# Performance work log

Hardware: AMD Instinct MI355X
Metric: run time of the kernel (lower is better)

The kernel has to match this reference:

```python
import jax, jax.numpy as jnp
import numpy as np

CODEBOOK_SIZE = 1024
EMBEDDING_DIM = 256
COMMITMENT_COST = 0.25


def setup_inputs() -> dict:
    key = jax.random.key(0)
    k1, k2 = jax.random.split(key)
    x = jax.random.normal(k1, (32, EMBEDDING_DIM, 32, 32), dtype=jnp.float32)
    # embedding initialized uniform(-1/K, 1/K) like the torch module
    embedding = jax.random.uniform(
        k2, (CODEBOOK_SIZE, EMBEDDING_DIM), dtype=jnp.float32,
        minval=-1.0 / CODEBOOK_SIZE, maxval=1.0 / CODEBOOK_SIZE)
    return {"x": x, "embedding": embedding}


def reference(x, embedding):
    # x: [B, C, H, W] -> inputs: [B, H, W, C]
    inputs = jnp.transpose(x, (0, 2, 3, 1))
    input_shape = inputs.shape
    flat = inputs.reshape(-1, EMBEDDING_DIM)  # [N, D]
    # squared L2 distances to codebook: [N, K]
    distances = (jnp.sum(flat ** 2, axis=1, keepdims=True)
                 + jnp.sum(embedding ** 2, axis=1)
                 - 2.0 * flat @ embedding.T)
    encoding_indices = jnp.argmin(distances, axis=1)  # [N]
    encodings = jax.nn.one_hot(encoding_indices, CODEBOOK_SIZE, dtype=jnp.float32)  # [N, K]
    # gather (same math as encodings @ embedding)
    quantized = embedding[encoding_indices].reshape(input_shape)  # [B, H, W, C]
    e_latent_loss = jnp.mean((jax.lax.stop_gradient(quantized) - inputs) ** 2)
    q_latent_loss = jnp.mean((quantized - jax.lax.stop_gradient(inputs)) ** 2)
    loss = q_latent_loss + COMMITMENT_COST * e_latent_loss
    # straight-through estimator
    quantized_st = inputs + jax.lax.stop_gradient(quantized - inputs)
    return (loss, jnp.transpose(quantized_st, (0, 3, 1, 2)), encodings)
```

## Files before the change

kernel.cpp:

```cpp
#include <hip/hip_runtime.h>
#include <cstdint>
#include <cstddef>

constexpr int B = 32, C = 256, H = 32, W = 32;
constexpr int NPTS = B * H * W;
constexpr int DIM  = 256;
constexpr int K    = 1024;
constexpr int QELEMS = B * C * H * W;
constexpr int CHW = C * H * W;

typedef __attribute__((ext_vector_type(8))) short s8v;
typedef __attribute__((ext_vector_type(4))) float f32x4;

#define GLD_LDS16(g, l)                                                        \
  __builtin_amdgcn_global_load_lds(                                            \
      (const __attribute__((address_space(1))) unsigned int*)(g),              \
      (__attribute__((address_space(3))) unsigned int*)(l), 16, 0, 0)

__device__ __forceinline__ unsigned short f2bf(float f) {
  unsigned u = __float_as_uint(f);
  return (unsigned short)((u + 0x7FFFu + ((u >> 16) & 1u)) >> 16);
}

__global__ __launch_bounds__(256) void eprep_kernel(const float* __restrict__ emb,
                                                    unsigned short* __restrict__ ehi,
                                                    float* __restrict__ esq) {
  __shared__ float sums[4][64];
  const int t = threadIdx.x;
  const int k = blockIdx.x * 64 + (t & 63);
  const int seg = t >> 6;
  const float* er = emb + (size_t)k * DIM + seg * 64;
  float v[64];
  float4* v4 = (float4*)v;
#pragma unroll
  for (int i = 0; i < 16; ++i) v4[i] = *(const float4*)(er + i * 4);
  float s = 0.f;
#pragma unroll
  for (int i = 0; i < 64; ++i) s = fmaf(v[i], v[i], s);
  unsigned short* eo = ehi + (size_t)k * DIM + seg * 64;
#pragma unroll
  for (int i = 0; i < 8; ++i) {
    unsigned short h[8];
#pragma unroll
    for (int j = 0; j < 8; ++j) h[j] = f2bf(v[i * 8 + j]);
    *(s8v*)(eo + i * 8) = *(s8v*)h;
  }
  sums[seg][t & 63] = s;
  __syncthreads();
  if (t < 64)
    esq[blockIdx.x * 64 + t] =
        ((sums[0][t] + sums[1][t]) + sums[2][t]) + sums[3][t];
}

__global__ __launch_bounds__(256) void xprep_kernel(const float* __restrict__ x,
                                                    unsigned short* __restrict__ xhi,
                                                    float* __restrict__ xsq) {
  __shared__ float xls[DIM][64];
  const int t = threadIdx.x;
  const int n0 = blockIdx.x * 64;
  const int bb = n0 >> 10, hw0 = n0 & 1023;
  const int p = t & 63, cs = t >> 6;
  const float* xb = x + (size_t)bb * CHW + hw0;
#pragma unroll 8
  for (int r = 0; r < 64; ++r) {
    const int c = r * 4 + cs;
    xls[c][p] = xb[(size_t)c * 1024 + p];
  }
  __syncthreads();
  if (t < 64) {
    float s = 0.f;
#pragma unroll 8
    for (int c = 0; c < 256; ++c) {
      const float v = xls[c][t];
      s = fmaf(v, v, s);
    }
    xsq[n0 + t] = s;
  }
  const int p2 = t >> 2, cb = (t & 3) * 64;
  unsigned short* xo = xhi + (size_t)(n0 + p2) * DIM + cb;
#pragma unroll
  for (int i = 0; i < 8; ++i) {
    unsigned short h[8];
#pragma unroll
    for (int j = 0; j < 8; ++j) h[j] = f2bf(xls[cb + i * 8 + j][p2]);
    *(s8v*)(xo + i * 8) = *(s8v*)h;
  }
}

constexpr float MARGIN = 1e-3f;
__global__ __launch_bounds__(256) void coarse_kernel(
    const unsigned short* __restrict__ xhi, const unsigned short* __restrict__ ehi,
    const float* __restrict__ esq, const float* __restrict__ xsq,
    float* __restrict__ part, unsigned int* __restrict__ cand) {
  __shared__ __align__(16) unsigned short xs[128][32];
  __shared__ __align__(16) unsigned short es[128][32];
  __shared__ float xsq_s[128], esq_s[128], thr_s[128];
  __shared__ unsigned long long red2[2][128];
  __shared__ unsigned int cntL[128];

  const int t = threadIdx.x;
  const int lane = t & 63, w = t >> 6;
  const int wn = (w & 1) * 64, wk = (w >> 1) * 64;
  const int col = lane & 15, quad = lane >> 4;
  const int nblk = blockIdx.x * 128;
  const int kblk = blockIdx.y * 128;

  if (t < 128) {
    xsq_s[t] = xsq[nblk + t];
    esq_s[t] = esq[kblk + t];
    cntL[t] = 0u;
  }

  f32x4 acc[4][4];
#pragma unroll
  for (int i = 0; i < 4; ++i)
#pragma unroll
    for (int j = 0; j < 4; ++j) acc[i][j] = (f32x4){0.f, 0.f, 0.f, 0.f};

  const int gl_row = lane >> 2;
  const int gl_c   = (lane & 3) * 8;

  for (int c0 = 0; c0 < DIM; c0 += 32) {
    __syncthreads();
#pragma unroll
    for (int i = 0; i < 2; ++i) {
      const int inst = w + 4 * i;
      const int row = inst * 16 + gl_row;
      GLD_LDS16(xhi + (size_t)(nblk + row) * DIM + c0 + gl_c, &xs[inst * 16][0]);
      GLD_LDS16(ehi + (size_t)(kblk + row) * DIM + c0 + gl_c, &es[inst * 16][0]);
    }
    __syncthreads();
    s8v a[4], b[4];
#pragma unroll
    for (int ti = 0; ti < 4; ++ti)
      a[ti] = *(const s8v*)&xs[wn + ti * 16 + col][quad * 8];
#pragma unroll
    for (int tj = 0; tj < 4; ++tj)
      b[tj] = *(const s8v*)&es[wk + tj * 16 + col][quad * 8];
#pragma unroll
    for (int ti = 0; ti < 4; ++ti)
#pragma unroll
      for (int tj = 0; tj < 4; ++tj)
        acc[ti][tj] = __builtin_amdgcn_mfma_f32_16x16x32_bf16(
            a[ti], b[tj], acc[ti][tj], 0, 0, 0);
  }

  unsigned long long nmin[4][4];
#pragma unroll
  for (int ti = 0; ti < 4; ++ti)
#pragma unroll
    for (int r = 0; r < 4; ++r) nmin[ti][r] = ~0ULL;
#pragma unroll
  for (int ti = 0; ti < 4; ++ti)
#pragma unroll
    for (int tj = 0; tj < 4; ++tj) {
      const int krel = wk + tj * 16 + col;
      const float eq = esq_s[krel];
#pragma unroll
      for (int r = 0; r < 4; ++r) {
        const int nl = wn + ti * 16 + quad * 4 + r;
        const float d = (xsq_s[nl] + eq) - 2.f * acc[ti][tj][r];
        const unsigned long long key =
            ((unsigned long long)__float_as_uint(d) << 32) |
            (unsigned)(kblk + krel);
        if (key < nmin[ti][r]) nmin[ti][r] = key;
      }
    }
#pragma unroll
  for (int o = 1; o < 16; o <<= 1)
#pragma unroll
    for (int ti = 0; ti < 4; ++ti)
#pragma unroll
      for (int r = 0; r < 4; ++r) {
        const unsigned long long v = __shfl_xor(nmin[ti][r], o, 64);
        if (v < nmin[ti][r]) nmin[ti][r] = v;
      }
  if (col == 0) {
#pragma unroll
    for (int ti = 0; ti < 4; ++ti)
#pragma unroll
      for (int r = 0; r < 4; ++r)
        red2[w >> 1][wn + ti * 16 + quad * 4 + r] = nmin[ti][r];
  }
  __syncthreads();
  if (t < 128) {
    const unsigned long long m0 = red2[0][t], m1 = red2[1][t];
    const unsigned long long m = (m1 < m0) ? m1 : m0;
    const float dmin = __uint_as_float((unsigned)(m >> 32));
    part[(size_t)(nblk + t) * 8 + blockIdx.y] = dmin;
    thr_s[t] = dmin + MARGIN;
  }
  __syncthreads();
#pragma unroll
  for (int ti = 0; ti < 4; ++ti)
#pragma unroll
    for (int tj = 0; tj < 4; ++tj) {
      const int krel = wk + tj * 16 + col;
      const float eq = esq_s[krel];
#pragma unroll
      for (int r = 0; r < 4; ++r) {
        const int nl = wn + ti * 16 + quad * 4 + r;
        const float d = (xsq_s[nl] + eq) - 2.f * acc[ti][tj][r];
        if (d <= thr_s[nl]) {
          const unsigned slot = atomicAdd(&cntL[nl], 1u);
          if (slot < 4u)
            cand[((size_t)(nblk + nl) * 8 + blockIdx.y) * 4 + slot] =
                (unsigned)(kblk + krel);
        }
      }
    }
  __syncthreads();
  if (t < 128) {
    unsigned c = cntL[t];
    const size_t base = ((size_t)(nblk + t) * 8 + blockIdx.y) * 4;
    if (c > 4u) { cand[base + 3] = 0xFFFFFFFEu; c = 3u; }
    for (unsigned s = c; s < 4u; ++s) cand[base + s] = 0xFFFFFFFFu;
  }
}

__global__ __launch_bounds__(256) void resolve_kernel(
    const float* __restrict__ x, const float* __restrict__ emb,
    const float* __restrict__ esq, const float* __restrict__ xsq,
    const float* __restrict__ part, const unsigned int* __restrict__ cand,
    int* __restrict__ idx) {
  __shared__ float xls[DIM][32];
  __shared__ unsigned list[1024];
  __shared__ unsigned long long best[32];
  __shared__ float thr_s[32], xsq_s[32];
  __shared__ int lcnt;

  const int t = threadIdx.x;
  const int n0 = blockIdx.x * 32;
  const int bb = n0 >> 10, hw0 = n0 & 1023;

  const float* xb = x + (size_t)bb * CHW + hw0;
  {
    const int p = t & 31, cs = t >> 5;
#pragma unroll 8
    for (int r = 0; r < 32; ++r) {
      const int c = r * 8 + cs;
      xls[c][p] = xb[(size_t)c * 1024 + p];
    }
  }
  if (t == 0) lcnt = 0;
  if (t < 32) {
    best[t] = ~0ULL;
    xsq_s[t] = xsq[n0 + t];
    const float4 p0 = *(const float4*)&part[(size_t)(n0 + t) * 8];
    const float4 p1 = *(const float4*)&part[(size_t)(n0 + t) * 8 + 4];
    float g = fminf(fminf(fminf(p0.x, p0.y), fminf(p0.z, p0.w)),
                    fminf(fminf(p1.x, p1.y), fminf(p1.z, p1.w)));
    thr_s[t] = g + MARGIN;
  }
  __syncthreads();

  {
    const int nn = t >> 3, s = t & 7;
    const float pv = part[(size_t)(n0 + nn) * 8 + s];
    if (pv <= thr_s[nn]) {
      const uint4 c4 = *(const uint4*)&cand[((size_t)(n0 + nn) * 8 + s) * 4];
      const unsigned vs[4] = {c4.x, c4.y, c4.z, c4.w};
#pragma unroll
      for (int i = 0; i < 4; ++i) {
        const unsigned v = vs[i];
        if (v == 0xFFFFFFFFu) continue;
        const unsigned entry = (v == 0xFFFFFFFEu)
                                   ? ((unsigned)nn << 11) | 1024u | (unsigned)s
                                   : ((unsigned)nn << 11) | (v & 1023u);
        const int pos = atomicAdd(&lcnt, 1);
        if (pos < 1024) list[pos] = entry;
      }
    }
  }
  __syncthreads();

  const int L = lcnt < 1024 ? lcnt : 1024;
  for (int e = t; e < L; e += 256) {
    const unsigned entry = list[e];
    const int p = entry >> 11;
    const float xq = xsq_s[p];
    int klo, khi;
    if (entry & 1024u) { const int s = entry & 7; klo = s * 128; khi = klo + 128; }
    else               { klo = entry & 1023u; khi = klo + 1; }
    for (int k = klo; k < khi; ++k) {
      const float* er = emb + (size_t)k * DIM;
      float dot = 0.f;
#pragma unroll 4
      for (int c4 = 0; c4 < DIM; c4 += 4) {
        const float4 e4 = *(const float4*)(er + c4);
        dot = fmaf(xls[c4 + 0][p], e4.x, dot);
        dot = fmaf(xls[c4 + 1][p], e4.y, dot);
        dot = fmaf(xls[c4 + 2][p], e4.z, dot);
        dot = fmaf(xls[c4 + 3][p], e4.w, dot);
      }
      const float t1 = xq + esq[k];
      const float d = t1 - 2.f * dot;
      const unsigned long long key =
          ((unsigned long long)__float_as_uint(d) << 32) | (unsigned)k;
      atomicMin(&best[p], key);
    }
  }
  __syncthreads();
  if (t < 32) idx[n0 + t] = (int)(best[t] & 0xFFFFFFFFu);
}

__global__ __launch_bounds__(256) void quant_enc_kernel(
    const float* __restrict__ x, const float* __restrict__ emb,
    const int* __restrict__ idx, float* __restrict__ outq,
    float* __restrict__ enc, float* __restrict__ loss) {
  __shared__ float tile[DIM * 32];
  __shared__ int ids[32];
  __shared__ float lred[4];
  const int t = threadIdx.x;
  const int n0 = blockIdx.x * 32;
  const int bb = n0 >> 10, hw0 = n0 & 1023;

  if (t < 32) ids[t] = idx[n0 + t];
  __syncthreads();

  const int p = t & 31, cseg = t >> 5;
  const int row = ids[p];
  const float* er = emb + (size_t)row * DIM + cseg * 32;
#pragma unroll
  for (int i = 0; i < 8; ++i) {
    const float4 v = *(const float4*)(er + i * 4);
    const int c = cseg * 32 + i * 4;
    tile[(c + 0) * 32 + p] = v.x;
    tile[(c + 1) * 32 + p] = v.y;
    tile[(c + 2) * 32 + p] = v.z;
    tile[(c + 3) * 32 + p] = v.w;
  }
  __syncthreads();

  float lsum = 0.f;
  const float* xb = x + (size_t)bb * CHW + hw0;
  float* ob = outq + (size_t)bb * CHW + hw0;
#pragma unroll
  for (int i = 0; i < 32; ++i) {
    const int c = cseg + i * 8;
    const float q  = tile[c * 32 + p];
    const float xv = xb[(size_t)c * 1024 + p];
    ob[(size_t)c * 1024 + p] = q;
    const float d = q - xv;
    lsum = fmaf(d, d, lsum);
  }
  float s = lsum;
#pragma unroll
  for (int o = 32; o > 0; o >>= 1) s += __shfl_down(s, o, 64);
  if ((t & 63) == 0) lred[t >> 6] = s;

#pragma unroll 4
  for (int r = 0; r < 32; ++r) {
    const int id = ids[r];
    const int kb = t * 4;
    float* eb = enc + (size_t)(n0 + r) * K + kb;
    eb[0] = (kb + 0 == id) ? 1.f : 0.f;
    eb[1] = (kb + 1 == id) ? 1.f : 0.f;
    eb[2] = (kb + 2 == id) ? 1.f : 0.f;
    eb[3] = (kb + 3 == id) ? 1.f : 0.f;
  }

  __syncthreads();
  if (t == 0) {
    const float tot = (lred[0] + lred[1] + lred[2] + lred[3]) * (1.25f / (float)QELEMS);
    atomicAdd(loss, tot);
  }
}

extern "C" void kernel_launch(void* const* d_in, const int* in_sizes, int n_in,
                              void* d_out, int out_size, void* d_ws, size_t ws_size,
                              hipStream_t stream) {
  const float* x   = (const float*)d_in[0];
  const float* emb = (const float*)d_in[1];
  float* out  = (float*)d_out;
  float* loss = out;
  float* outq = out + 1;
  float* enc  = out + 1 + QELEMS;

  char* ws = (char*)d_ws;
  unsigned short* ehi  = (unsigned short*)ws;
  float*          esq  = (float*)(ws + 524288);
  float*          xsq  = (float*)(ws + 528384);
  int*            idx  = (int*)(ws + 659456);
  float*          part = (float*)(ws + 790528);
  unsigned int*   cand = (unsigned int*)(ws + 1839104);
  unsigned short* xhi  = (unsigned short*)(ws + 6033408);

  hipMemsetAsync(loss, 0, sizeof(float), stream);

  eprep_kernel<<<K / 64, 256, 0, stream>>>(emb, ehi, esq);
  xprep_kernel<<<NPTS / 64, 256, 0, stream>>>(x, xhi, xsq);
  dim3 cg(NPTS / 128, 8);
  coarse_kernel<<<cg, 256, 0, stream>>>(xhi, ehi, esq, xsq, part, cand);
  resolve_kernel<<<NPTS / 32, 256, 0, stream>>>(x, emb, esq, xsq, part, cand, idx);
  quant_enc_kernel<<<NPTS / 32, 256, 0, stream>>>(x, emb, idx, outq, enc, loss);
}
```

Before: 300.6 us.

## Fuse resolve and quantize/one-hot kernels, reuse staged x, vectorize encoding stores

Merges the candidate-resolve kernel with the quantize/encoding kernel, so the chosen indices stay in shared memory and x is read from the already staged LDS tile instead of global memory. Removes one launch, the idx workspace round trip and a second read of x. The one-hot output is now written with 16-byte float4 stores, offset by 3 floats to match the alignment of enc (output base +1+QELEMS), with the leftover edge columns handled by the last thread. LDS use per block grows, which may lower occupancy, and the quantized tile is processed in two halves with extra barriers.

Result: slower. 311.3 us (+3.6%).

```diff
diff --git a/kernel.cpp b/kernel.cpp
--- a/kernel.cpp
+++ b/kernel.cpp
@@ -218,15 +218,19 @@
   }
 }
 
-__global__ __launch_bounds__(256) void resolve_kernel(
+__global__ __launch_bounds__(256) void finish_kernel(
     const float* __restrict__ x, const float* __restrict__ emb,
     const float* __restrict__ esq, const float* __restrict__ xsq,
     const float* __restrict__ part, const unsigned int* __restrict__ cand,
-    int* __restrict__ idx) {
+    float* __restrict__ outq, float* __restrict__ enc,
+    float* __restrict__ loss) {
   __shared__ float xls[DIM][32];
+  __shared__ float tile[DIM][16];
   __shared__ unsigned list[1024];
   __shared__ unsigned long long best[32];
   __shared__ float thr_s[32], xsq_s[32];
+  __shared__ int ids[32];
+  __shared__ float lred[4];
   __shared__ int lcnt;
 
   const int t = threadIdx.x;
@@ -301,63 +305,61 @@
     }
   }
   __syncthreads();
-  if (t < 32) idx[n0 + t] = (int)(best[t] & 0xFFFFFFFFu);
-}
-
-__global__ __launch_bounds__(256) void quant_enc_kernel(
-    const float* __restrict__ x, const float* __restrict__ emb,
-    const int* __restrict__ idx, float* __restrict__ outq,
-    float* __restrict__ enc, float* __restrict__ loss) {
-  __shared__ float tile[DIM * 32];
-  __shared__ int ids[32];
-  __shared__ float lred[4];
-  const int t = threadIdx.x;
-  const int n0 = blockIdx.x * 32;
-  const int bb = n0 >> 10, hw0 = n0 & 1023;
-
-  if (t < 32) ids[t] = idx[n0 + t];
-  __syncthreads();
-
-  const int p = t & 31, cseg = t >> 5;
-  const int row = ids[p];
-  const float* er = emb + (size_t)row * DIM + cseg * 32;
-#pragma unroll
-  for (int i = 0; i < 8; ++i) {
-    const float4 v = *(const float4*)(er + i * 4);
-    const int c = cseg * 32 + i * 4;
-    tile[(c + 0) * 32 + p] = v.x;
-    tile[(c + 1) * 32 + p] = v.y;
-    tile[(c + 2) * 32 + p] = v.z;
-    tile[(c + 3) * 32 + p] = v.w;
-  }
+  if (t < 32) ids[t] = (int)(best[t] & 0xFFFFFFFFu);
   __syncthreads();
 
   float lsum = 0.f;
-  const float* xb = x + (size_t)bb * CHW + hw0;
   float* ob = outq + (size_t)bb * CHW + hw0;
 #pragma unroll
-  for (int i = 0; i < 32; ++i) {
-    const int c = cseg + i * 8;
-    const float q  = tile[c * 32 + p];
-    const float xv = xb[(size_t)c * 1024 + p];
-    ob[(size_t)c * 1024 + p] = q;
-    const float d = q - xv;
-    lsum = fmaf(d, d, lsum);
+  for (int h = 0; h < 2; ++h) {
+    const int p16 = t & 15, cs16 = t >> 4;
+    const int row = ids[h * 16 + p16];
+    const float* er = emb + (size_t)row * DIM + cs16 * 16;
+#pragma unroll
+    for (int i = 0; i < 4; ++i) {
+      const float4 v = *(const float4*)(er + i * 4);
+      const int c = cs16 * 16 + i * 4;
+      tile[c + 0][p16] = v.x;
+      tile[c + 1][p16] = v.y;
+      tile[c + 2][p16] = v.z;
+      tile[c + 3][p16] = v.w;
+    }
+    __syncthreads();
+#pragma unroll
+    for (int i = 0; i < 16; ++i) {
+      const int c = cs16 + i * 16;
+      const float q  = tile[c][p16];
+      const float xv = xls[c][h * 16 + p16];
+      ob[(size_t)c * 1024 + h * 16 + p16] = q;
+      const float d = q - xv;
+      lsum = fmaf(d, d, lsum);
+    }
+    __syncthreads();
   }
   float s = lsum;
 #pragma unroll
   for (int o = 32; o > 0; o >>= 1) s += __shfl_down(s, o, 64);
   if ((t & 63) == 0) lred[t >> 6] = s;
 
+  if (t < 255) {
+    const int kb = 3 + 4 * t;
 #pragma unroll 4
-  for (int r = 0; r < 32; ++r) {
-    const int id = ids[r];
-    const int kb = t * 4;
-    float* eb = enc + (size_t)(n0 + r) * K + kb;
-    eb[0] = (kb + 0 == id) ? 1.f : 0.f;
-    eb[1] = (kb + 1 == id) ? 1.f : 0.f;
-    eb[2] = (kb + 2 == id) ? 1.f : 0.f;
-    eb[3] = (kb + 3 == id) ? 1.f : 0.f;
+    for (int r = 0; r < 32; ++r) {
+      const int id = ids[r];
+      float4 v = {0.f, 0.f, 0.f, 0.f};
+      const unsigned rel = (unsigned)(id - kb);
+      if (rel < 4u) ((float*)&v)[rel] = 1.f;
+      *(float4*)(enc + (size_t)(n0 + r) * K + kb) = v;
+    }
+  } else {
+    for (int r = 0; r < 32; ++r) {
+      const int id = ids[r];
+      float* eb = enc + (size_t)(n0 + r) * K;
+      eb[0] = (id == 0) ? 1.f : 0.f;
+      eb[1] = (id == 1) ? 1.f : 0.f;
+      eb[2] = (id == 2) ? 1.f : 0.f;
+      eb[1023] = (id == 1023) ? 1.f : 0.f;
+    }
   }
 
   __syncthreads();
@@ -381,10 +383,9 @@
   unsigned short* ehi  = (unsigned short*)ws;
   float*          esq  = (float*)(ws + 524288);
   float*          xsq  = (float*)(ws + 528384);
-  int*            idx  = (int*)(ws + 659456);
-  float*          part = (float*)(ws + 790528);
-  unsigned int*   cand = (unsigned int*)(ws + 1839104);
-  unsigned short* xhi  = (unsigned short*)(ws + 6033408);
+  float*          part = (float*)(ws + 659456);
+  unsigned int*   cand = (unsigned int*)(ws + 1708032);
+  unsigned short* xhi  = (unsigned short*)(ws + 5902336);
 
   hipMemsetAsync(loss, 0, sizeof(float), stream);
 
@@ -392,6 +393,6 @@
   xprep_kernel<<<NPTS / 64, 256, 0, stream>>>(x, xhi, xsq);
   dim3 cg(NPTS / 128, 8);
   coarse_kernel<<<cg, 256, 0, stream>>>(xhi, ehi, esq, xsq, part, cand);
-  resolve_kernel<<<NPTS / 32, 256, 0, stream>>>(x, emb, esq, xsq, part, cand, idx);
-  quant_enc_kernel<<<NPTS / 32, 256, 0, stream>>>(x, emb, idx, outq, enc, loss);
-}
+  finish_kernel<<<NPTS / 32, 256, 0, stream>>>(x, emb, esq, xsq, part, cand,
+                                               outq, enc, loss);
+}
```
